# Optimization experiments

Hardware: AMD Instinct MI355X
Metric: run time of the kernel (lower is better)

Reference implementation:

```python
import jax, jax.numpy as jnp
import numpy as np

FP4_MAX = 6.0
FP8_MAX = 448.0  # float8_e4m3fn max
BLOCK = 16
# representable |values| of fp4 e2m1 and decision midpoints (ties round up)
FP4_LEVELS = jnp.array([0.0, 0.5, 1.0, 1.5, 2.0, 3.0, 4.0, 6.0], dtype=jnp.float32)
FP4_MIDS = jnp.array([0.25, 0.75, 1.25, 1.75, 2.5, 3.5, 5.0], dtype=jnp.float32)


def _fp4_round(x):
    # round to nearest fp4 e2m1 value (magnitudes clamp at 6)
    a = jnp.abs(x)
    idx = jnp.searchsorted(FP4_MIDS, a, side='right')
    return jnp.sign(x) * FP4_LEVELS[idx]


def nvfp4_quant(x, global_scale):
    # x: [M, K] float32 -> (q_fp4 values [M, K], block scales [M, K//16] fp8-representable)
    M, K = x.shape
    xb = x.reshape(M, K // BLOCK, BLOCK)
    block_amax = jnp.max(jnp.abs(xb), axis=-1)  # [M, K//16]
    scale = jnp.clip(block_amax * (global_scale / FP4_MAX), 0.0, FP8_MAX)
    scale = scale.astype(jnp.float8_e4m3fn).astype(jnp.float32)
    safe = jnp.where(scale == 0.0, 1.0, scale)
    q = _fp4_round(xb * (global_scale / safe)[..., None])
    return q.reshape(M, K), scale


def setup_inputs() -> dict:
    key = jax.random.key(0)
    k_in, k_w, k_b = jax.random.split(key, 3)
    M, K, N = 256, 5120, 13824
    x = jax.random.normal(k_in, (M, K), dtype=jnp.float32)
    # build pre-quantized NVFP4 weight buffers (as the module's load_quantized_weights would)
    w = jax.random.normal(k_w, (N, K), dtype=jnp.float32) * 0.02
    w_gs = (FP8_MAX * FP4_MAX) / jnp.max(jnp.abs(w))  # scalar float32
    w_fp4, w_scale = nvfp4_quant(w, w_gs)
    bias = jax.random.normal(k_b, (N,), dtype=jnp.float32) * 0.01
    return {
        'input': x,
        'weight_fp4': w_fp4,            # [N, K] fp4 values held in f32
        'weight_scale': w_scale,        # [N, K//16] fp8_e4m3-representable f32
        'weight_global_scale': w_gs,    # scalar f32
        'bias': bias,                   # [N]
    }


def reference(input, weight_fp4, weight_scale, weight_global_scale, bias):
    # activations cast to bf16 (as in the torch module), math in f32
    x = input.astype(jnp.bfloat16).astype(jnp.float32)
    M, K = x.shape
    N = weight_fp4.shape[0]
    # per-tensor global scale for activations
    a_gs = (FP8_MAX * FP4_MAX) / jnp.max(jnp.abs(x))
    alpha = 1.0 / (a_gs * weight_global_scale)
    # on-the-fly fp4 quantization of activations
    a_fp4, a_scale = nvfp4_quant(x, a_gs)
    # block-scaled dequant-matmul: out = (a_fp4*s_a) @ (w_fp4*s_w)^T * alpha + bias
    a_u = (a_fp4.reshape(M, K // BLOCK, BLOCK) * a_scale[..., None]).reshape(M, K)
    w_u = (weight_fp4.reshape(N, K // BLOCK, BLOCK) * weight_scale[..., None]).reshape(N, K)
    out = jnp.einsum('mk,nk->mn', a_u, w_u) * alpha + bias[None, :]
    return out
```

## Files before the change

### kernel.cpp

```cpp
#include <hip/hip_runtime.h>

typedef __attribute__((ext_vector_type(8))) __bf16 bf16x8;
typedef __attribute__((ext_vector_type(4))) float floatx4;

#define M_TOT 256
#define K_TOT 5120
#define N_TOT 13824
#define NBLK  320
#define BN    128
#define KSPLIT 4
#define KCH   1280
#define KSUP  256
#define NSUP  5

#define GLOAD_LDS16(g, l)                                                     \
  __builtin_amdgcn_global_load_lds(                                           \
      (const __attribute__((address_space(1))) void*)(g),                     \
      (__attribute__((address_space(3))) void*)(l), 16, 0, 0)

static __device__ __forceinline__ float bf16r(float v) { return (float)(__bf16)v; }

static __device__ __forceinline__ float fp4round(float v) {
  float a = fabsf(v), q;
  if      (a < 0.25f) q = 0.0f;
  else if (a < 0.75f) q = 0.5f;
  else if (a < 1.25f) q = 1.0f;
  else if (a < 1.75f) q = 1.5f;
  else if (a < 2.5f)  q = 2.0f;
  else if (a < 3.5f)  q = 3.0f;
  else if (a < 5.0f)  q = 4.0f;
  else                q = 6.0f;
  return copysignf(q, v);
}

static __device__ __forceinline__ float cvt_e4m3(float f) {
  if (f < 0.015625f) return rintf(f * 512.0f) * 0.001953125f;
  int e = (int)(__float_as_uint(f) >> 23) - 127;
  float q = __uint_as_float((unsigned)(e - 3 + 127) << 23);
  return rintf(f / q) * q;
}

__global__ void k_prep(const float* __restrict__ x, unsigned* __restrict__ amax_bits,
                       float4* __restrict__ out4) {
  int idx = blockIdx.x * blockDim.x + threadIdx.x;
#pragma unroll 1
  for (int j = idx; j < 884736; j += 327680) out4[j] = (float4){0.f, 0.f, 0.f, 0.f};
  float4 v = ((const float4*)x)[idx];
  float m = fmaxf(fmaxf(fabsf(bf16r(v.x)), fabsf(bf16r(v.y))),
                  fmaxf(fabsf(bf16r(v.z)), fabsf(bf16r(v.w))));
#pragma unroll
  for (int off = 32; off; off >>= 1) m = fmaxf(m, __shfl_xor(m, off));
  if ((threadIdx.x & 63) == 0) atomicMax(amax_bits, __float_as_uint(m));
}

__global__ void k_aquant(const float* __restrict__ x,
                         const unsigned* __restrict__ amax_bits,
                         __bf16* __restrict__ au) {
  int idx = blockIdx.x * blockDim.x + threadIdx.x;
  int m = idx / NBLK;
  int b = idx - m * NBLK;
  float amax = __uint_as_float(*amax_bits);
  float gs  = 2688.0f / amax;
  float gs6 = gs / 6.0f;
  const float4* xp = (const float4*)(x + m * K_TOT + b * 16);
  float4 v0 = xp[0], v1 = xp[1], v2 = xp[2], v3 = xp[3];
  float xv[16];
  xv[0]=bf16r(v0.x); xv[1]=bf16r(v0.y); xv[2]=bf16r(v0.z); xv[3]=bf16r(v0.w);
  xv[4]=bf16r(v1.x); xv[5]=bf16r(v1.y); xv[6]=bf16r(v1.z); xv[7]=bf16r(v1.w);
  xv[8]=bf16r(v2.x); xv[9]=bf16r(v2.y); xv[10]=bf16r(v2.z); xv[11]=bf16r(v2.w);
  xv[12]=bf16r(v3.x); xv[13]=bf16r(v3.y); xv[14]=bf16r(v3.z); xv[15]=bf16r(v3.w);
  float am = 0.f;
#pragma unroll
  for (int j = 0; j < 16; ++j) am = fmaxf(am, fabsf(xv[j]));
  float s = cvt_e4m3(fminf(am * gs6, 448.0f));
  float g = gs / ((s == 0.f) ? 1.f : s);
  bf16x8 p0, p1;
#pragma unroll
  for (int j = 0; j < 8; ++j) p0[j] = (__bf16)(fp4round(xv[j] * g) * s);
#pragma unroll
  for (int j = 0; j < 8; ++j) p1[j] = (__bf16)(fp4round(xv[8 + j] * g) * s);
  bf16x8* dst = (bf16x8*)(au + (size_t)idx * 16);
  dst[0] = p0; dst[1] = p1;
}

__global__ __launch_bounds__(1024, 4) void k_gemm(
    const __bf16* __restrict__ au,
    const float*  __restrict__ w,
    const float*  __restrict__ wsc,
    const unsigned* __restrict__ amax_bits,
    const float*  __restrict__ wgs,
    const float*  __restrict__ bias,
    float* __restrict__ out)
{
  __shared__ __bf16 Ab[M_TOT * KSUP];

  const int tid  = threadIdx.x;
  const int lane = tid & 63;
  const int wv   = tid >> 6;
  const int wm   = wv >> 3;
  const int wn   = wv & 7;

  const int s     = blockIdx.x & 3;
  const int n0    = (blockIdx.x >> 2) * BN;
  const int kbase = s * KCH;

  const int hi  = lane >> 4;
  const int r15 = lane & 15;
  const int xo  = r15 & 7;

  const int arow0 = tid >> 5;
  const int achk  = (tid & 31) ^ ((tid >> 5) & 7);
  const __bf16* asrc0 = au + (size_t)arow0 * K_TOT + kbase + achk * 8;

  const int nrow = n0 + wn * 16 + r15;
  const float* wrow  = w   + (size_t)nrow * K_TOT + kbase + hi * 8;
  const float* wsrow = wsc + (size_t)nrow * NBLK + s * (KCH / 16);
  const int hi2 = hi >> 1;

  const int abase = (wm * 128 + r15) * 512;
  const int cof0  = ((0 * 4 + hi) ^ xo) << 4;
  const int cof1  = ((1 * 4 + hi) ^ xo) << 4;

  floatx4 acc[8];
#pragma unroll
  for (int fm = 0; fm < 8; ++fm) acc[fm] = (floatx4){0.f, 0.f, 0.f, 0.f};

  struct WSlot { float4 a, b, c, d; float s0, s1; };
  WSlot sA, sB;

  auto issueA = [&](int c) {
    const __bf16* src = asrc0 + c * KSUP;
    char* dst = (char*)Ab + tid * 16;
#pragma unroll
    for (int i = 0; i < 8; ++i)
      GLOAD_LDS16(src + (size_t)i * 32 * K_TOT, dst + i * 16384);
  };
  auto issueW = [&](WSlot& sl, int t) {
    const float* p = wrow + t * 64;
    sl.a = *(const float4*)(p);
    sl.b = *(const float4*)(p + 4);
    sl.c = *(const float4*)(p + 32);
    sl.d = *(const float4*)(p + 36);
    sl.s0 = wsrow[t * 4 + hi2];
    sl.s1 = wsrow[t * 4 + 2 + hi2];
  };
  auto cvt8 = [](float4 x, float4 y, float sc) {
    bf16x8 r;
    r[0] = (__bf16)(x.x * sc); r[1] = (__bf16)(x.y * sc);
    r[2] = (__bf16)(x.z * sc); r[3] = (__bf16)(x.w * sc);
    r[4] = (__bf16)(y.x * sc); r[5] = (__bf16)(y.y * sc);
    r[6] = (__bf16)(y.z * sc); r[7] = (__bf16)(y.w * sc);
    return r;
  };
  auto stepC = [&](WSlot& sl, int j, int tre) {
    bf16x8 b0 = cvt8(sl.a, sl.b, sl.s0);
    bf16x8 b1 = cvt8(sl.c, sl.d, sl.s1);
    if (tre >= 0) issueW(sl, tre);
    const char* pA = (const char*)Ab + abase + j * 128;
#pragma unroll
    for (int fm = 0; fm < 8; ++fm) {
      bf16x8 af = *(const bf16x8*)(pA + fm * 8192 + cof0);
      acc[fm] = __builtin_amdgcn_mfma_f32_16x16x32_bf16(af, b0, acc[fm], 0, 0, 0);
    }
#pragma unroll
    for (int fm = 0; fm < 8; ++fm) {
      bf16x8 af = *(const bf16x8*)(pA + fm * 8192 + cof1);
      acc[fm] = __builtin_amdgcn_mfma_f32_16x16x32_bf16(af, b1, acc[fm], 0, 0, 0);
    }
  };

#pragma unroll 1
  for (int c = 0; c < NSUP; ++c) {
    const int tb = c * 4;
    if (c > 0) {
      asm volatile("s_waitcnt lgkmcnt(0)" ::: "memory");
      __builtin_amdgcn_sched_barrier(0);
      __builtin_amdgcn_s_barrier();
      __builtin_amdgcn_sched_barrier(0);
    }
    issueA(c);
    __builtin_amdgcn_sched_barrier(0);
    issueW(sA, tb + 0);
    issueW(sB, tb + 1);
    asm volatile("s_waitcnt vmcnt(8)" ::: "memory");
    __builtin_amdgcn_sched_barrier(0);
    __builtin_amdgcn_s_barrier();
    __builtin_amdgcn_sched_barrier(0);
    stepC(sA, 0, tb + 2);
    stepC(sB, 1, tb + 3);
    stepC(sA, 2, -1);
    stepC(sB, 3, -1);
  }

  float amax = __uint_as_float(*amax_bits);
  float a_gs = 2688.0f / amax;
  float alpha = 1.0f / (a_gs * wgs[0]);
  const int ncol = n0 + wn * 16 + r15;
  const float bb = (s == 0) ? bias[ncol] : 0.0f;
#pragma unroll
  for (int fm = 0; fm < 8; ++fm) {
    int mrow = wm * 128 + fm * 16 + hi * 4;
#pragma unroll
    for (int j = 0; j < 4; ++j)
      atomicAdd(&out[(size_t)(mrow + j) * N_TOT + ncol],
                acc[fm][j] * alpha + bb);
  }
}

extern "C" void kernel_launch(void* const* d_in, const int* in_sizes, int n_in,
                              void* d_out, int out_size, void* d_ws, size_t ws_size,
                              hipStream_t stream) {
  const float* x    = (const float*)d_in[0];
  const float* wq   = (const float*)d_in[1];
  const float* wsc  = (const float*)d_in[2];
  const float* wgs  = (const float*)d_in[3];
  const float* bias = (const float*)d_in[4];
  float* out = (float*)d_out;

  unsigned* amax = (unsigned*)d_ws;
  __bf16* au = (__bf16*)((char*)d_ws + 256);

  hipMemsetAsync(d_ws, 0, 4, stream);
  k_prep<<<dim3(1280), dim3(256), 0, stream>>>(x, amax, (float4*)out);
  k_aquant<<<dim3(M_TOT * NBLK / 256), dim3(256), 0, stream>>>(x, amax, au);
  k_gemm<<<dim3((N_TOT / BN) * KSPLIT), dim3(1024), 0, stream>>>(au, wq, wsc, amax, wgs, bias, out);
}
```

Measured before the change: 248.2 us.

## Double-buffer activation tiles in LDS and prefetch next chunk during MFMA

Halves the activation K-chunk held in LDS and allocates two buffers, so the next chunk's global-to-LDS load is issued before the MFMAs on the current chunk. The original waited at a barrier at the start of each chunk with no overlap. Weight registers now hold four single-K32 slots prefetched four steps ahead, and the XOR swizzle is re-derived for the 256-byte row stride. The change doubles the barrier count and shortens each step's compute, which could reduce MFMA density between synchronisations.

```diff
diff --git a/kernel.cpp b/kernel.cpp
--- a/kernel.cpp
+++ b/kernel.cpp
@@ -10,8 +10,9 @@
 #define BN    128
 #define KSPLIT 4
 #define KCH   1280
-#define KSUP  256
-#define NSUP  5
+#define KSUP  128
+#define NSUP  10
+#define NSTEP 40
 
 #define GLOAD_LDS16(g, l)                                                     \
   __builtin_amdgcn_global_load_lds(                                           \
@@ -92,7 +93,7 @@
     const float*  __restrict__ bias,
     float* __restrict__ out)
 {
-  __shared__ __bf16 Ab[M_TOT * KSUP];
+  __shared__ __bf16 Ab[2][M_TOT * KSUP];
 
   const int tid  = threadIdx.x;
   const int lane = tid & 63;
@@ -106,90 +107,79 @@
 
   const int hi  = lane >> 4;
   const int r15 = lane & 15;
-  const int xo  = r15 & 7;
-
-  const int arow0 = tid >> 5;
-  const int achk  = (tid & 31) ^ ((tid >> 5) & 7);
-  const __bf16* asrc0 = au + (size_t)arow0 * K_TOT + kbase + achk * 8;
+
+  const int arow0 = wv * 16 + hi;
+  const int l15   = lane & 15;
 
   const int nrow = n0 + wn * 16 + r15;
-  const float* wrow  = w   + (size_t)nrow * K_TOT + kbase + hi * 8;
-  const float* wsrow = wsc + (size_t)nrow * NBLK + s * (KCH / 16);
+  const float* wrow = w   + (size_t)nrow * K_TOT + kbase + hi * 8;
+  const float* wsp  = wsc + (size_t)nrow * NBLK + s * (KCH / 16);
   const int hi2 = hi >> 1;
 
-  const int abase = (wm * 128 + r15) * 512;
-  const int cof0  = ((0 * 4 + hi) ^ xo) << 4;
-  const int cof1  = ((1 * 4 + hi) ^ xo) << 4;
-
   floatx4 acc[8];
 #pragma unroll
   for (int fm = 0; fm < 8; ++fm) acc[fm] = (floatx4){0.f, 0.f, 0.f, 0.f};
 
-  struct WSlot { float4 a, b, c, d; float s0, s1; };
-  WSlot sA, sB;
-
-  auto issueA = [&](int c) {
-    const __bf16* src = asrc0 + c * KSUP;
-    char* dst = (char*)Ab + tid * 16;
-#pragma unroll
-    for (int i = 0; i < 8; ++i)
-      GLOAD_LDS16(src + (size_t)i * 32 * K_TOT, dst + i * 16384);
+  struct Slot { float4 a, b; float sc; };
+  Slot w0, w1, w2, w3;
+
+  auto issueA = [&](int c, int buf) {
+    char* dst = (char*)(&Ab[buf][0]) + wv * 4096;
+#pragma unroll
+    for (int i = 0; i < 4; ++i) {
+      const int row = arow0 + i * 4;
+      const int g   = l15 ^ (row & 15);
+      const __bf16* src = au + (size_t)row * K_TOT + kbase + c * KSUP + g * 8;
+      GLOAD_LDS16(src, dst + i * 1024);
+    }
   };
-  auto issueW = [&](WSlot& sl, int t) {
-    const float* p = wrow + t * 64;
-    sl.a = *(const float4*)(p);
-    sl.b = *(const float4*)(p + 4);
-    sl.c = *(const float4*)(p + 32);
-    sl.d = *(const float4*)(p + 36);
-    sl.s0 = wsrow[t * 4 + hi2];
-    sl.s1 = wsrow[t * 4 + 2 + hi2];
+  auto issueW = [&](Slot& sl, int t) {
+    const float* p = wrow + t * 32;
+    sl.a  = *(const float4*)p;
+    sl.b  = *(const float4*)(p + 4);
+    sl.sc = wsp[t * 2 + hi2];
   };
-  auto cvt8 = [](float4 x, float4 y, float sc) {
-    bf16x8 r;
-    r[0] = (__bf16)(x.x * sc); r[1] = (__bf16)(x.y * sc);
-    r[2] = (__bf16)(x.z * sc); r[3] = (__bf16)(x.w * sc);
-    r[4] = (__bf16)(y.x * sc); r[5] = (__bf16)(y.y * sc);
-    r[6] = (__bf16)(y.z * sc); r[7] = (__bf16)(y.w * sc);
-    return r;
+  auto stepC = [&](Slot& sl, int buf, int j, int tnext) {
+    bf16x8 bfr;
+    bfr[0] = (__bf16)(sl.a.x * sl.sc); bfr[1] = (__bf16)(sl.a.y * sl.sc);
+    bfr[2] = (__bf16)(sl.a.z * sl.sc); bfr[3] = (__bf16)(sl.a.w * sl.sc);
+    bfr[4] = (__bf16)(sl.b.x * sl.sc); bfr[5] = (__bf16)(sl.b.y * sl.sc);
+    bfr[6] = (__bf16)(sl.b.z * sl.sc); bfr[7] = (__bf16)(sl.b.w * sl.sc);
+    if (tnext < NSTEP) issueW(sl, tnext);
+    const char* pA = (const char*)(&Ab[buf][0]) + (wm * 128 + r15) * 256;
+#pragma unroll
+    for (int fm = 0; fm < 8; ++fm) {
+      bf16x8 af = *(const bf16x8*)(pA + fm * 4096 + (((j * 4 + hi) ^ r15) << 4));
+      acc[fm] = __builtin_amdgcn_mfma_f32_16x16x32_bf16(af, bfr, acc[fm], 0, 0, 0);
+    }
   };
-  auto stepC = [&](WSlot& sl, int j, int tre) {
-    bf16x8 b0 = cvt8(sl.a, sl.b, sl.s0);
-    bf16x8 b1 = cvt8(sl.c, sl.d, sl.s1);
-    if (tre >= 0) issueW(sl, tre);
-    const char* pA = (const char*)Ab + abase + j * 128;
-#pragma unroll
-    for (int fm = 0; fm < 8; ++fm) {
-      bf16x8 af = *(const bf16x8*)(pA + fm * 8192 + cof0);
-      acc[fm] = __builtin_amdgcn_mfma_f32_16x16x32_bf16(af, b0, acc[fm], 0, 0, 0);
-    }
-#pragma unroll
-    for (int fm = 0; fm < 8; ++fm) {
-      bf16x8 af = *(const bf16x8*)(pA + fm * 8192 + cof1);
-      acc[fm] = __builtin_amdgcn_mfma_f32_16x16x32_bf16(af, b1, acc[fm], 0, 0, 0);
-    }
-  };
+
+  issueA(0, 0);
+  __builtin_amdgcn_sched_barrier(0);
+  issueW(w0, 0); issueW(w1, 1); issueW(w2, 2); issueW(w3, 3);
+  asm volatile("s_waitcnt vmcnt(12)" ::: "memory");
+  __builtin_amdgcn_sched_barrier(0);
+  __builtin_amdgcn_s_barrier();
+  __builtin_amdgcn_sched_barrier(0);
 
 #pragma unroll 1
   for (int c = 0; c < NSUP; ++c) {
+    const int buf = c & 1;
     const int tb = c * 4;
-    if (c > 0) {
-      asm volatile("s_waitcnt lgkmcnt(0)" ::: "memory");
+    if (c + 1 < NSUP) {
+      issueA(c + 1, buf ^ 1);
+      __builtin_amdgcn_sched_barrier(0);
+    }
+    stepC(w0, buf, 0, tb + 4);
+    stepC(w1, buf, 1, tb + 5);
+    stepC(w2, buf, 2, tb + 6);
+    stepC(w3, buf, 3, tb + 7);
+    if (c + 1 < NSUP) {
+      asm volatile("s_waitcnt vmcnt(12) lgkmcnt(0)" ::: "memory");
       __builtin_amdgcn_sched_barrier(0);
       __builtin_amdgcn_s_barrier();
       __builtin_amdgcn_sched_barrier(0);
     }
-    issueA(c);
-    __builtin_amdgcn_sched_barrier(0);
-    issueW(sA, tb + 0);
-    issueW(sB, tb + 1);
-    asm volatile("s_waitcnt vmcnt(8)" ::: "memory");
-    __builtin_amdgcn_sched_barrier(0);
-    __builtin_amdgcn_s_barrier();
-    __builtin_amdgcn_sched_barrier(0);
-    stepC(sA, 0, tb + 2);
-    stepC(sB, 1, tb + 3);
-    stepC(sA, 2, -1);
-    stepC(sB, 3, -1);
   }
 
   float amax = __uint_as_float(*amax_bits);
```

Result: no change. 246.9 us (-0.5%).
